# Performance work log

Measured on AMD Instinct MI355X. Metric: run time of the kernel, lower is better.

The kernel has to match this reference:

```python
import jax, jax.numpy as jnp
import numpy as np

B, S, D, H, DH, F = 2, 2048, 1024, 16, 64, 4096
EPS = 1e-5


def layernorm(x, gamma, beta):
    mu = jnp.mean(x, axis=-1, keepdims=True)
    var = jnp.mean((x - mu) ** 2, axis=-1, keepdims=True)
    return (x - mu) * jax.lax.rsqrt(var + EPS) * gamma + beta


def setup_inputs() -> dict:
    key = jax.random.key(0)
    ks = jax.random.split(key, 13)
    sc = 0.02
    return {
        "x": jax.random.normal(ks[0], (B, S, D), jnp.float32),
        "W_Q": jax.random.normal(ks[1], (H, DH, D), jnp.float32) * sc,  # per-head [d_head, d_model]
        "W_K": jax.random.normal(ks[2], (H, DH, D), jnp.float32) * sc,
        "W_V": jax.random.normal(ks[3], (H, DH, D), jnp.float32) * sc,
        "W_O": jax.random.normal(ks[4], (H * DH, D), jnp.float32) * sc,
        "W_up": jax.random.normal(ks[5], (D, F), jnp.float32) * sc,
        "b_up": jax.random.normal(ks[6], (F,), jnp.float32) * sc,
        "W_down": jax.random.normal(ks[7], (F, D), jnp.float32) * sc,
        "b_down": jax.random.normal(ks[8], (D,), jnp.float32) * sc,
        "gamma_1": jnp.ones((D,), jnp.float32),
        "beta_1": jnp.zeros((D,), jnp.float32),
        "gamma_2": jnp.ones((D,), jnp.float32),
        "beta_2": jnp.zeros((D,), jnp.float32),
    }


def reference(x, W_Q, W_K, W_V, W_O, W_up, b_up, W_down, b_down, gamma_1, beta_1, gamma_2, beta_2):
    u = layernorm(x, gamma_1, beta_1)
    # per-head projections: input @ W.t() -> [B, H, S, DH]
    Q = jnp.einsum("bsd,hed->bhse", u, W_Q)
    K = jnp.einsum("bsd,hed->bhse", u, W_K)
    V = jnp.einsum("bsd,hed->bhse", u, W_V)
    # Faithful quirk: original does K.reshape(B, DH, S) (raw reshape, NOT transpose)
    K_r = K.reshape(B, H, DH, S)
    scores = jnp.matmul(Q, K_r) / D  # [B,H,S,S]; quirk: scaled by d_model, not sqrt(d_head)
    attn = jax.nn.softmax(scores, axis=-1)
    heads = jnp.matmul(attn, V)  # [B,H,S,DH]
    heads_cat = heads.transpose(0, 2, 1, 3).reshape(B, S, H * DH)  # concat heads on last dim
    z1 = x + heads_cat @ W_O
    v1 = layernorm(z1, gamma_2, beta_2)
    v3 = jax.nn.gelu(v1 @ W_up + b_up, approximate=False)
    z2 = z1 + v3 @ W_down + b_down
    return z2
```

## Files before the change

kernel.cpp:

```cpp
#include <hip/hip_runtime.h>
#include <hip/hip_bf16.h>


typedef __attribute__((ext_vector_type(8))) short short8v;
typedef __attribute__((ext_vector_type(4))) short short4v;
typedef __attribute__((ext_vector_type(4))) float f32x4;

__device__ __forceinline__ float b2f(unsigned short u) {
    unsigned int x = ((unsigned int)u) << 16;
    float f;
    __builtin_memcpy(&f, &x, 4);
    return f;
}
__device__ __forceinline__ unsigned short f2b(float f) {
    unsigned int x;
    __builtin_memcpy(&x, &f, 4);
    unsigned int r = (x + 0x7FFFu + ((x >> 16) & 1u)) >> 16;
    return (unsigned short)r;
}
__device__ __forceinline__ void gload16(const unsigned short* g, unsigned short* l) {
    __builtin_amdgcn_global_load_lds(
        (const __attribute__((address_space(1))) unsigned int*)g,
        (__attribute__((address_space(3))) unsigned int*)l, 16, 0, 0);
}
__device__ __forceinline__ bool is_f32(const unsigned int* flagp) {
    return *flagp == 0x3F800000u;
}

__global__ __launch_bounds__(256) void cast_qkv_k(const void* __restrict__ s0,
                                                  const void* __restrict__ s1,
                                                  const void* __restrict__ s2,
                                                  unsigned short* __restrict__ dst,
                                                  const unsigned int* __restrict__ flagp) {
    const bool f32 = is_f32(flagp);
    const int seg = blockIdx.x >> 9;
    const int i = ((blockIdx.x & 511) * 256 + threadIdx.x) * 8;
    const void* src = seg == 0 ? s0 : (seg == 1 ? s1 : s2);
    unsigned short* d = dst + (size_t)seg * 1048576 + i;
    if (f32) {
        const float* s = (const float*)src + i;
        float4 a = *(const float4*)s;
        float4 b = *(const float4*)(s + 4);
        union { unsigned short u[8]; int4 v; } o;
        o.u[0] = f2b(a.x); o.u[1] = f2b(a.y); o.u[2] = f2b(a.z); o.u[3] = f2b(a.w);
        o.u[4] = f2b(b.x); o.u[5] = f2b(b.y); o.u[6] = f2b(b.z); o.u[7] = f2b(b.w);
        *(int4*)d = o.v;
    } else {
        *(int4*)d = *(const int4*)((const unsigned short*)src + i);
    }
}

__global__ __launch_bounds__(256) void cast_small_k(const void* __restrict__ s0,
                                                    const void* __restrict__ s1,
                                                    const void* __restrict__ s2,
                                                    const void* __restrict__ s3,
                                                    const void* __restrict__ s4,
                                                    const void* __restrict__ s5,
                                                    unsigned short* __restrict__ dst,
                                                    const unsigned int* __restrict__ flagp) {
    const bool f32 = is_f32(flagp);
    const int seg = blockIdx.x < 2 ? 0 : blockIdx.x - 1;
    const void* srcs[6] = {s0, s1, s2, s3, s4, s5};
    const int offs[6] = {0, 4096, 5120, 6144, 7168, 8192};
    const int lens[6] = {4096, 1024, 1024, 1024, 1024, 1024};
    const int base = (blockIdx.x < 2 ? blockIdx.x * 2048 : 0);
    const int i = base + threadIdx.x * 8;
    if (i >= lens[seg]) return;
    const void* src = srcs[seg];
    unsigned short* d = dst + offs[seg] + i;
    if (f32) {
        const float* s = (const float*)src + i;
        float4 a = *(const float4*)s;
        float4 b = *(const float4*)(s + 4);
        union { unsigned short u[8]; int4 v; } o;
        o.u[0] = f2b(a.x); o.u[1] = f2b(a.y); o.u[2] = f2b(a.z); o.u[3] = f2b(a.w);
        o.u[4] = f2b(b.x); o.u[5] = f2b(b.y); o.u[6] = f2b(b.z); o.u[7] = f2b(b.w);
        *(int4*)d = o.v;
    } else {
        *(int4*)d = *(const int4*)((const unsigned short*)src + i);
    }
}

__global__ __launch_bounds__(256) void castT_k(const void* __restrict__ src,
                                               unsigned short* __restrict__ dst,
                                               int rows, int cols,
                                               const unsigned int* __restrict__ flagp) {
    const bool f32 = is_f32(flagp);
    __shared__ float tile[32][33];
    const int t = threadIdx.x, tx = t & 31, ty = t >> 5;
    const int c0 = blockIdx.x * 32, r0 = blockIdx.y * 32;
#pragma unroll
    for (int i = 0; i < 4; i++) {
        int r = r0 + ty + i * 8;
        float v;
        if (f32) v = ((const float*)src)[(size_t)r * cols + c0 + tx];
        else     v = b2f(((const unsigned short*)src)[(size_t)r * cols + c0 + tx]);
        tile[ty + i * 8][tx] = v;
    }
    __syncthreads();
#pragma unroll
    for (int i = 0; i < 4; i++) {
        int c = c0 + ty + i * 8;
        dst[(size_t)c * rows + r0 + tx] = f2b(tile[tx][ty + i * 8]);
    }
}

__global__ __launch_bounds__(256) void initz_k(float* __restrict__ dst,
                                               const void* __restrict__ src,
                                               const unsigned int* __restrict__ flagp) {
    const int i = (blockIdx.x * 256 + threadIdx.x) * 4;
    if (is_f32(flagp)) {
        *(float4*)(dst + i) = *(const float4*)((const float*)src + i);
    } else {
        uint2 v = *(const uint2*)((const unsigned short*)src + i);
        float4 o;
        o.x = b2f((unsigned short)(v.x & 0xffff));
        o.y = b2f((unsigned short)(v.x >> 16));
        o.z = b2f((unsigned short)(v.y & 0xffff));
        o.w = b2f((unsigned short)(v.y >> 16));
        *(float4*)(dst + i) = o;
    }
}
__global__ __launch_bounds__(256) void fin_k(const float* __restrict__ src,
                                             void* __restrict__ dst,
                                             const unsigned short* __restrict__ bias,
                                             const unsigned int* __restrict__ flagp) {
    const bool f32 = is_f32(flagp);
    const int i = (blockIdx.x * 256 + threadIdx.x) * 4;
    float4 v = *(const float4*)(src + i);
    int c = i & 1023;
    v.x += b2f(bias[c]); v.y += b2f(bias[c + 1]);
    v.z += b2f(bias[c + 2]); v.w += b2f(bias[c + 3]);
    if (f32) {
        *(float4*)((float*)dst + i) = v;
    } else {
        union { unsigned short u[4]; uint2 q; } o;
        o.u[0] = f2b(v.x); o.u[1] = f2b(v.y); o.u[2] = f2b(v.z); o.u[3] = f2b(v.w);
        *(uint2*)((unsigned short*)dst + i) = o.q;
    }
}

template <int MODE>
__global__ __launch_bounds__(256) void ln_k(const void* __restrict__ inp,
                                            unsigned short* __restrict__ outp,
                                            const unsigned short* __restrict__ gamma,
                                            const unsigned short* __restrict__ beta,
                                            const unsigned int* __restrict__ flagp) {
    const int row = blockIdx.x, t = threadIdx.x;
    float xv[4];
    bool f32 = (MODE == 1) ? true : is_f32(flagp);
    if (f32) {
        const float* p = (const float*)inp + (size_t)row * 1024 + t * 4;
        float4 v = *(const float4*)p;
        xv[0] = v.x; xv[1] = v.y; xv[2] = v.z; xv[3] = v.w;
    } else {
        const unsigned short* p = (const unsigned short*)inp + (size_t)row * 1024 + t * 4;
        uint2 v = *(const uint2*)p;
        xv[0] = b2f((unsigned short)(v.x & 0xffff));
        xv[1] = b2f((unsigned short)(v.x >> 16));
        xv[2] = b2f((unsigned short)(v.y & 0xffff));
        xv[3] = b2f((unsigned short)(v.y >> 16));
    }
    float s = xv[0] + xv[1] + xv[2] + xv[3];
    float q = xv[0] * xv[0] + xv[1] * xv[1] + xv[2] * xv[2] + xv[3] * xv[3];
#pragma unroll
    for (int off = 32; off >= 1; off >>= 1) {
        s += __shfl_xor(s, off);
        q += __shfl_xor(q, off);
    }
    __shared__ float ls[8];
    if ((t & 63) == 0) { ls[t >> 6] = s; ls[4 + (t >> 6)] = q; }
    __syncthreads();
    s = ls[0] + ls[1] + ls[2] + ls[3];
    q = ls[4] + ls[5] + ls[6] + ls[7];
    const float mu = s * (1.f / 1024.f);
    const float rs = rsqrtf(q * (1.f / 1024.f) - mu * mu + 1e-5f);
    union { unsigned short u[4]; uint2 v; } o;
#pragma unroll
    for (int i = 0; i < 4; i++) {
        int c = t * 4 + i;
        o.u[i] = f2b((xv[i] - mu) * rs * b2f(gamma[c]) + b2f(beta[c]));
    }
    *(uint2*)(outp + (size_t)row * 1024 + t * 4) = o.v;
}

template <int EPI>
__global__ __launch_bounds__(256) void gemm_k(const unsigned short* __restrict__ A,
                                              const unsigned short* __restrict__ Bm,
                                              unsigned short* __restrict__ C,
                                              unsigned short* __restrict__ C2,
                                              unsigned short* __restrict__ C3,
                                              const unsigned short* __restrict__ bias,
                                              float* __restrict__ outf,
                                              int N, int ldk, int tilesM, int tilesN,
                                              int kLen) {
    __shared__ unsigned short As[128 * 32];
    __shared__ unsigned short Bs[128 * 32];
    const int t = threadIdx.x;
    const int w = t >> 6, lane = t & 63, ln = t & 15, quad = (t & 63) >> 4;
    const int wm = w >> 1, wn = w & 1;
    const int bm = blockIdx.x % tilesM;
    const int bn = (blockIdx.x / tilesM) % tilesN;
    const int kc = blockIdx.x / (tilesM * tilesN);
    const int m0 = bm << 7, n0 = bn << 7;
    const int k0 = kc * kLen;
    f32x4 acc[4][4] = {};

    const int srow = lane >> 2;
    const int scol = (lane & 3) << 3;

    for (int kt = k0; kt < k0 + kLen; kt += 32) {
        __syncthreads();
#pragma unroll
        for (int r = 0; r < 2; r++) {
            const int blk = r * 4 + w;
            const int row = blk * 16 + srow;
            gload16(&A[(size_t)(m0 + row) * ldk + kt + scol], &As[blk * 512]);
            gload16(&Bm[(size_t)(n0 + row) * ldk + kt + scol], &Bs[blk * 512]);
        }
        asm volatile("s_waitcnt vmcnt(0)" ::: "memory");
        __syncthreads();
        short8v af[4], bfv[4];
#pragma unroll
        for (int mi = 0; mi < 4; mi++)
            af[mi] = *(const short8v*)&As[(wm * 64 + mi * 16 + ln) * 32 + quad * 8];
#pragma unroll
        for (int nj = 0; nj < 4; nj++)
            bfv[nj] = *(const short8v*)&Bs[(wn * 64 + nj * 16 + ln) * 32 + quad * 8];
#pragma unroll
        for (int mi = 0; mi < 4; mi++)
#pragma unroll
            for (int nj = 0; nj < 4; nj++)
                acc[mi][nj] = __builtin_amdgcn_mfma_f32_16x16x32_bf16(
                    af[mi], bfv[nj], acc[mi][nj], 0, 0, 0);
    }

#pragma unroll
    for (int mi = 0; mi < 4; mi++) {
#pragma unroll
        for (int nj = 0; nj < 4; nj++) {
#pragma unroll
            for (int r = 0; r < 4; r++) {
                const int m = m0 + wm * 64 + mi * 16 + quad * 4 + r;
                const int n = n0 + wn * 64 + nj * 16 + ln;
                float v = acc[mi][nj][r];
                if (EPI == 4) {
                    float x = v + b2f(bias[n]);
                    C[(size_t)m * N + n] = f2b(0.5f * x * (1.f + erff(x * 0.70710678118654752f)));
                } else if (EPI == 6) {
                    int b = m >> 11, s = m & 2047;
                    int seg = n >> 10, nn = n & 1023, h = nn >> 6, e = nn & 63;
                    if (seg == 0) {
                        C[(size_t)m * 1024 + nn] = f2b(v);
                    } else if (seg == 1) {
                        C2[((size_t)((b * 16 + h) * 2048 + (s & 31) * 64 + e)) * 64 + (s >> 5)] = f2b(v);
                    } else {
                        C3[((size_t)((b * 16 + h) * 64 + e)) * 2048 + s] = f2b(v);
                    }
                } else {
                    unsafeAtomicAdd(&outf[(size_t)m * N + n], v);
                }
            }
        }
    }
}

__global__ __launch_bounds__(512, 4) void attn_k(const unsigned short* __restrict__ Q,
                                                 const unsigned short* __restrict__ Kt,
                                                 const unsigned short* __restrict__ Vt,
                                                 unsigned short* __restrict__ Hd) {
    __shared__ unsigned short Ks[2][2][128 * 32];
    __shared__ unsigned short Vs[2][64 * 128];
    const int t = threadIdx.x;
    const int w = t >> 6, l = t & 63, ln = t & 15, quad = (t & 63) >> 4;
    const int qt = blockIdx.x & 15, bh = blockIdx.x >> 4;
    const int b = bh >> 4, h = bh & 15;
    const int i0 = qt << 7;

    short8v aq[2];
    {
        const unsigned short* qp =
            Q + ((size_t)(b * 2048 + i0 + w * 16 + ln)) * 1024 + h * 64 + quad * 8;
        aq[0] = *(const short8v*)qp;
        aq[1] = *(const short8v*)(qp + 32);
    }

    const size_t kbase = (size_t)bh * (2048 * 64);
    const size_t vbase = (size_t)bh * (64 * 2048);

    size_t ksrc[2]; int klds[2];
    size_t vsrc[2]; int vlds[2];
#pragma unroll
    for (int r = 0; r < 2; r++) {
        int idx2 = w * 2 + r;
        int ksp = idx2 & 1, J = idx2 >> 1;
        ksrc[r] = (size_t)(J * 16 + (l >> 2)) * 64 + ksp * 32 + (l & 3) * 8;
        klds[r] = ksp * 4096 + J * 512;
        int c = idx2;
        int e = c * 4 + (l >> 4), pp = l & 15;
        int g = (pp & 8) | ((pp & 7) ^ (e & 7));
        vsrc[r] = (size_t)e * 2048 + g * 8;
        vlds[r] = c * 512;
    }

#pragma unroll
    for (int r = 0; r < 2; r++) {
        gload16(Kt + kbase + ksrc[r], &Ks[0][0][0] + klds[r]);
        gload16(Vt + vbase + vsrc[r], &Vs[0][0] + vlds[r]);
    }

    f32x4 O[4] = {};
    float lsum = 0.f;
    int cur = 0;
    const float sc = 9.765625e-4f;

    for (int jt = 0; jt < 16; jt++) {
        asm volatile("s_waitcnt vmcnt(0)" ::: "memory");
        __syncthreads();
        if (jt < 15) {
            const size_t j1 = (size_t)(jt + 1) << 7;
#pragma unroll
            for (int r = 0; r < 2; r++) {
                gload16(Kt + kbase + j1 * 64 + ksrc[r], &Ks[cur ^ 1][0][0] + klds[r]);
                gload16(Vt + vbase + j1 + vsrc[r], &Vs[cur ^ 1][0] + vlds[r]);
            }
        }

        f32x4 S[8] = {};
#pragma unroll
        for (int ks = 0; ks < 2; ks++) {
#pragma unroll
            for (int nj = 0; nj < 8; nj++) {
                short8v bk = *(const short8v*)&Ks[cur][ks][(nj * 16 + ln) * 32 + quad * 8];
                S[nj] = __builtin_amdgcn_mfma_f32_16x16x32_bf16(bk, aq[ks], S[nj], 0, 0, 0);
            }
        }
        short4v pk[8];
#pragma unroll
        for (int nj = 0; nj < 8; nj++) {
            union { unsigned short u[4]; short4v v; } pu;
#pragma unroll
            for (int r = 0; r < 4; r++) {
                float p = __expf(S[nj][r] * sc);
                lsum += p;
                pu.u[r] = f2b(p);
            }
            pk[nj] = pu.v;
        }
#pragma unroll
        for (int nj = 0; nj < 8; nj++) {
            int g = 2 * nj + (quad >> 1);
            int pos = (g & 8) | ((g & 7) ^ (ln & 7));
            int off = pos * 8 + (quad & 1) * 4;
#pragma unroll
            for (int ne = 0; ne < 4; ne++) {
                short4v bv = *(const short4v*)&Vs[cur][(ne * 16 + ln) * 128 + off];
                O[ne] = __builtin_amdgcn_mfma_f32_16x16x16bf16_1k(pk[nj], bv, O[ne], 0, 0, 0);
            }
        }
        cur ^= 1;
    }

    lsum += __shfl_xor(lsum, 16);
    lsum += __shfl_xor(lsum, 32);

#pragma unroll
    for (int r = 0; r < 4; r++) {
        float lr = __shfl(lsum, quad * 4 + r);
        float inv = 1.f / lr;
#pragma unroll
        for (int ne = 0; ne < 4; ne++) {
            int i = i0 + w * 16 + quad * 4 + r;
            int e = ne * 16 + ln;
            Hd[((size_t)(b * 2048 + i)) * 1024 + h * 64 + e] = f2b(O[ne][r] * inv);
        }
    }
}

extern "C" void kernel_launch(void* const* d_in, const int* in_sizes, int n_in,
                              void* d_out, int out_size, void* d_ws, size_t ws_size,
                              hipStream_t stream) {
    const unsigned int* flagp = (const unsigned int*)d_in[9];

    unsigned short* p = (unsigned short*)d_ws;
    unsigned short* Wqkv  = p; p += 3145728;
    unsigned short* WOt   = p; p += 1048576;
    unsigned short* Wupt  = p; p += 4194304;
    unsigned short* Wdnt  = p; p += 4194304;
    unsigned short* smallv = p; p += 9216;
    unsigned short* u     = p; p += 4194304;
    unsigned short* Qc    = p; p += 4194304;
    unsigned short* Ktt   = p; p += 4194304;
    unsigned short* Vtt   = p; p += 4194304;
    unsigned short* hd    = p; p += 4194304;
    float*          z1    = (float*)p;
    unsigned short* bupc = smallv;
    unsigned short* bdnc = smallv + 4096;
    unsigned short* g1c  = smallv + 5120;
    unsigned short* be1c = smallv + 6144;
    unsigned short* g2c  = smallv + 7168;
    unsigned short* be2c = smallv + 8192;
    unsigned short* v1   = u;
    unsigned short* v3   = Qc;

    dim3 blk(256);
    cast_qkv_k<<<1536, blk, 0, stream>>>(d_in[1], d_in[2], d_in[3], Wqkv, flagp);
    castT_k<<<dim3(32, 32),  blk, 0, stream>>>(d_in[4], WOt,  1024, 1024, flagp);
    castT_k<<<dim3(128, 32), blk, 0, stream>>>(d_in[5], Wupt, 1024, 4096, flagp);
    castT_k<<<dim3(32, 128), blk, 0, stream>>>(d_in[7], Wdnt, 4096, 1024, flagp);
    cast_small_k<<<7, blk, 0, stream>>>(d_in[6], d_in[8], d_in[9], d_in[10], d_in[11],
                                        d_in[12], smallv, flagp);

    ln_k<0><<<4096, blk, 0, stream>>>(d_in[0], u, g1c, be1c, flagp);
    gemm_k<6><<<768, blk, 0, stream>>>(u, Wqkv, Qc, Ktt, Vtt, nullptr, nullptr,
                                       3072, 1024, 32, 24, 1024);
    attn_k<<<512, dim3(512), 0, stream>>>(Qc, Ktt, Vtt, hd);
    initz_k<<<4096, blk, 0, stream>>>(z1, d_in[0], flagp);
    gemm_k<7><<<512, blk, 0, stream>>>(hd, WOt, nullptr, nullptr, nullptr, nullptr, z1,
                                       1024, 1024, 32, 8, 512);
    ln_k<1><<<4096, blk, 0, stream>>>(z1, v1, g2c, be2c, flagp);
    gemm_k<4><<<1024, blk, 0, stream>>>(v1, Wupt, v3, nullptr, nullptr, bupc, nullptr,
                                        4096, 1024, 32, 32, 1024);
    gemm_k<7><<<512, blk, 0, stream>>>(v3, Wdnt, nullptr, nullptr, nullptr, nullptr, z1,
                                       1024, 4096, 32, 8, 2048);
    fin_k<<<4096, blk, 0, stream>>>(z1, d_out, bdnc, flagp);
}
```

Measured before the change: 470.3 us.

## Replace atomic split-K accumulation with direct residual epilogue and bf16 partials

The output-projection GEMM drops split-K and writes z1 = x + acc directly in its epilogue, so the separate init kernel and the fp32 atomics go away. The down-projection keeps split-K by two, but each slice writes a bf16 partial into a scratch buffer that reuses the Wqkv region. The final kernel then sums both partials with z1 and the bias. This trades atomic traffic for plain stores, at the cost of half as many blocks for the O-projection and bf16 rounding of the partial sums.

```diff
diff --git a/kernel.cpp b/kernel.cpp
--- a/kernel.cpp
+++ b/kernel.cpp
@@ -105,32 +105,22 @@
     }
 }
 
-__global__ __launch_bounds__(256) void initz_k(float* __restrict__ dst,
-                                               const void* __restrict__ src,
-                                               const unsigned int* __restrict__ flagp) {
-    const int i = (blockIdx.x * 256 + threadIdx.x) * 4;
-    if (is_f32(flagp)) {
-        *(float4*)(dst + i) = *(const float4*)((const float*)src + i);
-    } else {
-        uint2 v = *(const uint2*)((const unsigned short*)src + i);
-        float4 o;
-        o.x = b2f((unsigned short)(v.x & 0xffff));
-        o.y = b2f((unsigned short)(v.x >> 16));
-        o.z = b2f((unsigned short)(v.y & 0xffff));
-        o.w = b2f((unsigned short)(v.y >> 16));
-        *(float4*)(dst + i) = o;
-    }
-}
 __global__ __launch_bounds__(256) void fin_k(const float* __restrict__ src,
+                                             const unsigned short* __restrict__ P0,
+                                             const unsigned short* __restrict__ P1,
                                              void* __restrict__ dst,
                                              const unsigned short* __restrict__ bias,
                                              const unsigned int* __restrict__ flagp) {
     const bool f32 = is_f32(flagp);
     const int i = (blockIdx.x * 256 + threadIdx.x) * 4;
     float4 v = *(const float4*)(src + i);
+    uint2 p0 = *(const uint2*)(P0 + i);
+    uint2 p1 = *(const uint2*)(P1 + i);
     int c = i & 1023;
-    v.x += b2f(bias[c]); v.y += b2f(bias[c + 1]);
-    v.z += b2f(bias[c + 2]); v.w += b2f(bias[c + 3]);
+    v.x += b2f(bias[c])     + b2f((unsigned short)(p0.x & 0xffff)) + b2f((unsigned short)(p1.x & 0xffff));
+    v.y += b2f(bias[c + 1]) + b2f((unsigned short)(p0.x >> 16))    + b2f((unsigned short)(p1.x >> 16));
+    v.z += b2f(bias[c + 2]) + b2f((unsigned short)(p0.y & 0xffff)) + b2f((unsigned short)(p1.y & 0xffff));
+    v.w += b2f(bias[c + 3]) + b2f((unsigned short)(p0.y >> 16))    + b2f((unsigned short)(p1.y >> 16));
     if (f32) {
         *(float4*)((float*)dst + i) = v;
     } else {
@@ -192,6 +182,8 @@
                                               unsigned short* __restrict__ C3,
                                               const unsigned short* __restrict__ bias,
                                               float* __restrict__ outf,
+                                              const void* __restrict__ xres,
+                                              const unsigned int* __restrict__ flagp,
                                               int N, int ldk, int tilesM, int tilesN,
                                               int kLen) {
     __shared__ unsigned short As[128 * 32];
@@ -235,6 +227,11 @@
                     af[mi], bfv[nj], acc[mi][nj], 0, 0, 0);
     }
 
+    bool xf32 = false;
+    if (EPI == 3) xf32 = is_f32(flagp);
+    unsigned short* Cp = C;
+    if (EPI == 8) Cp = C + (size_t)kc * 4194304;
+
 #pragma unroll
     for (int mi = 0; mi < 4; mi++) {
 #pragma unroll
@@ -244,7 +241,11 @@
                 const int m = m0 + wm * 64 + mi * 16 + quad * 4 + r;
                 const int n = n0 + wn * 64 + nj * 16 + ln;
                 float v = acc[mi][nj][r];
-                if (EPI == 4) {
+                if (EPI == 3) {
+                    float xv = xf32 ? ((const float*)xres)[(size_t)m * N + n]
+                                    : b2f(((const unsigned short*)xres)[(size_t)m * N + n]);
+                    outf[(size_t)m * N + n] = v + xv;
+                } else if (EPI == 4) {
                     float x = v + b2f(bias[n]);
                     C[(size_t)m * N + n] = f2b(0.5f * x * (1.f + erff(x * 0.70710678118654752f)));
                 } else if (EPI == 6) {
@@ -258,7 +259,7 @@
                         C3[((size_t)((b * 16 + h) * 64 + e)) * 2048 + s] = f2b(v);
                     }
                 } else {
-                    unsafeAtomicAdd(&outf[(size_t)m * N + n], v);
+                    Cp[(size_t)m * N + n] = f2b(v);
                 }
             }
         }
@@ -402,6 +403,7 @@
     unsigned short* be2c = smallv + 8192;
     unsigned short* v1   = u;
     unsigned short* v3   = Qc;
+    unsigned short* Pd   = Wqkv;
 
     dim3 blk(256);
     cast_qkv_k<<<1536, blk, 0, stream>>>(d_in[1], d_in[2], d_in[3], Wqkv, flagp);
@@ -413,15 +415,14 @@
 
     ln_k<0><<<4096, blk, 0, stream>>>(d_in[0], u, g1c, be1c, flagp);
     gemm_k<6><<<768, blk, 0, stream>>>(u, Wqkv, Qc, Ktt, Vtt, nullptr, nullptr,
-                                       3072, 1024, 32, 24, 1024);
+                                       nullptr, nullptr, 3072, 1024, 32, 24, 1024);
     attn_k<<<512, dim3(512), 0, stream>>>(Qc, Ktt, Vtt, hd);
-    initz_k<<<4096, blk, 0, stream>>>(z1, d_in[0], flagp);
-    gemm_k<7><<<512, blk, 0, stream>>>(hd, WOt, nullptr, nullptr, nullptr, nullptr, z1,
-                                       1024, 1024, 32, 8, 512);
+    gemm_k<3><<<256, blk, 0, stream>>>(hd, WOt, nullptr, nullptr, nullptr, nullptr, z1,
+                                       d_in[0], flagp, 1024, 1024, 32, 8, 1024);
     ln_k<1><<<4096, blk, 0, stream>>>(z1, v1, g2c, be2c, flagp);
     gemm_k<4><<<1024, blk, 0, stream>>>(v1, Wupt, v3, nullptr, nullptr, bupc, nullptr,
-                                        4096, 1024, 32, 32, 1024);
-    gemm_k<7><<<512, blk, 0, stream>>>(v3, Wdnt, nullptr, nullptr, nullptr, nullptr, z1,
-                                       1024, 4096, 32, 8, 2048);
-    fin_k<<<4096, blk, 0, stream>>>(z1, d_out, bdnc, flagp);
-}
+                                        nullptr, nullptr, 4096, 1024, 32, 32, 1024);
+    gemm_k<8><<<512, blk, 0, stream>>>(v3, Wdnt, Pd, nullptr, nullptr, nullptr, nullptr,
+                                       nullptr, nullptr, 1024, 4096, 32, 8, 2048);
+    fin_k<<<4096, blk, 0, stream>>>(z1, Pd, Pd + 4194304, d_out, bdnc, flagp);
+}
```

Result: faster. 449.8 us (-4.4%).
